# Kernel optimization log

Hardware: AMD Instinct MI355X
Metric: run time of the kernel (lower is better)

Reference implementation:

```python
import jax, jax.numpy as jnp
import numpy as np

NU, NI, D, E_MP, E_UI1, B = 40000, 40000, 128, 640000, 800000, 8192
N = NU + NI

def _segsum(x, ids, n):
    return jax.ops.segment_sum(x, ids, num_segments=n)

def _graph_conv(h, src, dst, n):
    # DGL GraphConv norm='both', weight=None: D_dst^{-1/2} A D_src^{-1/2} h, degrees clamped to >=1
    ones = jnp.ones(src.shape[0], h.dtype)
    outdeg = jnp.maximum(_segsum(ones, src, n), 1.0)
    indeg = jnp.maximum(_segsum(ones, dst, n), 1.0)
    hs = h * jax.lax.rsqrt(outdeg)[:, None]
    agg = _segsum(hs[src], dst, n)  # scatter-add over edges
    return agg * jax.lax.rsqrt(indeg)[:, None]

def _sem_att(z, W1, b1, W2):
    # z: [N, M, D]
    w = jnp.tanh(z @ W1 + b1) @ W2          # [N, M, 1]
    beta = jax.nn.softmax(w.mean(0), axis=0)  # [M, 1]
    return (beta[None] * z).sum(1)            # [N, D]

def _han3(h, mp_edges, W1, b1, W2):
    # 3 applications of the SAME HANLayer (2 metapaths), as in HGCL.forward
    for _ in range(3):
        z = jnp.stack([_graph_conv(h, s, d, h.shape[0]) for (s, d) in mp_edges], axis=1)
        h = _sem_att(z, W1, b1, W2)
    return h

def _ssl(d1, d2, idx):
    e1, e2 = d1[idx], d2[idx]
    n1 = e1 / jnp.maximum(jnp.linalg.norm(e1, axis=1, keepdims=True), 1e-12)
    n2 = e2 / jnp.maximum(jnp.linalg.norm(e2, axis=1, keepdims=True), 1e-12)
    pos = jnp.exp(jnp.sum(n1 * n2, axis=1) / 0.5)
    alls = jnp.sum(jnp.exp(n1 @ n2.T / 0.5), axis=1)
    return -jnp.sum(jnp.log(pos / alls)) / idx.shape[0]

def _layernorm(x, g, b):
    mu = x.mean(-1, keepdims=True)
    var = ((x - mu) ** 2).mean(-1, keepdims=True)
    return (x - mu) * jax.lax.rsqrt(var + 1e-5) * g + b

def setup_inputs():
    key = jax.random.key(0)
    ks = jax.random.split(key, 32)
    f = lambda k, sh, s: jax.random.normal(k, sh, jnp.float32) * s
    ri = lambda k, n, hi: jax.random.randint(k, (n,), 0, hi, dtype=jnp.int32)
    inp = {}
    inp['feat_user'] = f(ks[0], (NU, D), 0.05)
    inp['feat_item'] = f(ks[1], (NI, D), 0.05)
    inp['u_att_W1'] = f(ks[2], (D, 128), 0.05); inp['u_att_b1'] = jnp.zeros((128,), jnp.float32)
    inp['u_att_W2'] = f(ks[3], (128, 1), 0.05)
    inp['i_att_W1'] = f(ks[4], (D, 128), 0.05); inp['i_att_b1'] = jnp.zeros((128,), jnp.float32)
    inp['i_att_W2'] = f(ks[5], (128, 1), 0.05)
    inp['user_W'] = f(ks[6], (D, D), 0.05); inp['user_b'] = jnp.zeros((D,), jnp.float32)
    inp['item_W'] = f(ks[7], (D, D), 0.05); inp['item_b'] = jnp.zeros((D,), jnp.float32)
    inp['ln_g'] = jnp.ones((D,), jnp.float32); inp['ln_b'] = jnp.zeros((D,), jnp.float32)
    # metapath-reachable edge lists (user-user and item-item graphs)
    inp['u_mp0_src'] = ri(ks[8], E_MP, NU); inp['u_mp0_dst'] = ri(ks[9], E_MP, NU)
    inp['u_mp1_src'] = ri(ks[10], E_MP, NU); inp['u_mp1_dst'] = ri(ks[11], E_MP, NU)
    inp['i_mp0_src'] = ri(ks[12], E_MP, NI); inp['i_mp0_dst'] = ri(ks[13], E_MP, NI)
    inp['i_mp1_src'] = ri(ks[14], E_MP, NI); inp['i_mp1_dst'] = ri(ks[15], E_MP, NI)
    # symmetric UI adjacency in COO over N = NU + NI nodes
    ur = ri(ks[16], E_UI1, NU)
    ic = jax.random.randint(ks[17], (E_UI1,), NU, N, dtype=jnp.int32)
    inp['ui_row'] = jnp.concatenate([ur, ic])
    inp['ui_col'] = jnp.concatenate([ic, ur])
    # unique indices (torch.unique in ssl_loss is then a no-op up to ordering)
    inp['user_idx'] = jax.random.permutation(ks[18], NU)[:B]
    inp['item_idx'] = jax.random.permutation(ks[19], NI)[:B]
    inp['neg_item_idx'] = jax.random.permutation(ks[20], NI)[:B]
    return inp

def reference(feat_user, feat_item, u_att_W1, u_att_b1, u_att_W2, i_att_W1, i_att_b1, i_att_W2,
              user_W, user_b, item_W, item_b, ln_g, ln_b,
              u_mp0_src, u_mp0_dst, u_mp1_src, u_mp1_dst,
              i_mp0_src, i_mp0_dst, i_mp1_src, i_mp1_dst,
              ui_row, ui_col, user_idx, item_idx, neg_item_idx):
    h_u = _han3(feat_user, [(u_mp0_src, u_mp0_dst), (u_mp1_src, u_mp1_dst)], u_att_W1, u_att_b1, u_att_W2)
    h_i = _han3(feat_item, [(i_mp0_src, i_mp0_dst), (i_mp1_src, i_mp1_dst)], i_att_W1, i_att_b1, i_att_W2)
    vals = jnp.ones(ui_row.shape[0], jnp.float32)
    deg = _segsum(vals, ui_row, N)
    dinv = jnp.where(deg > 0, jax.lax.rsqrt(jnp.maximum(deg, 1e-30)), 0.0)
    w = dinv[ui_row] * dinv[ui_col]
    x = jnp.concatenate([feat_user, feat_item], axis=0)
    for _ in range(3):
        x = _segsum(w[:, None] * x[ui_col], ui_row, N)
    ui_u, ui_i = x[:NU], x[NU:]
    user_emb = 0.5 * h_u + 0.5 * ui_u
    item_emb = 0.5 * h_i + 0.5 * ui_i
    ssl_loss = 0.4 * _ssl(ui_u, user_emb, user_idx) + 0.4 * _ssl(ui_i, item_emb, item_idx)
    user_emb = _layernorm(jax.nn.relu(user_emb @ user_W + user_b), ln_g, ln_b)
    item_emb = _layernorm(jax.nn.relu(item_emb @ item_W + item_b), ln_g, ln_b)
    return (user_emb[user_idx], item_emb[item_idx], item_emb[neg_item_idx], ssl_loss)
```

## Files before the change

kernel.cpp:

```cpp
#include <hip/hip_runtime.h>
#include <math.h>

typedef unsigned short u16;
typedef unsigned int u32;
typedef unsigned char u8;
typedef __attribute__((ext_vector_type(8))) short bf16x8;
typedef __attribute__((ext_vector_type(4))) float f32x4;

#define CNU 40000
#define CNN 80000
#define CD  128
#define CEMP 640000
#define CEUI 1600000
#define CB  8192

#define BK_CAP 8064
#define P1_CHUNK 4096
#define NB_MP 157

__device__ __forceinline__ float bf2f(u16 b){
  union { u32 u; float f; } v; v.u = ((u32)b) << 16; return v.f;
}
__device__ __forceinline__ u16 f2bf(float f){
  union { float f; u32 u; } v; v.f = f;
  u32 u = v.u + 0x7FFFu + ((v.u >> 16) & 1u);
  return (u16)(u >> 16);
}
__device__ __forceinline__ float lo16f(u32 q){ union { u32 u; float f; } v; v.u = q << 16; return v.f; }
__device__ __forceinline__ float hi16f(u32 q){ union { u32 u; float f; } v; v.u = q & 0xFFFF0000u; return v.f; }

__global__ void k_zero(float* __restrict__ p, long long n){
  long long i = (long long)blockIdx.x*256 + threadIdx.x;
  if (i < n) p[i] = 0.f;
}

__global__ void k_izero(int* __restrict__ p, int n){
  int i = blockIdx.x*256 + threadIdx.x;
  if (i < n) p[i] = 0;
}

__global__ void k_initb(const float* __restrict__ fu, const float* __restrict__ fi,
                        u16* __restrict__ fb,
                        const float* __restrict__ Wu, const float* __restrict__ Wi,
                        u16* __restrict__ Wut, u16* __restrict__ Wit){
  int b = blockIdx.x;
  if (b < 40000){
    int idx = b*256 + threadIdx.x;
    float v = (idx < CNU*CD) ? fu[idx] : fi[idx - CNU*CD];
    fb[idx] = f2bf(v);
  } else {
    int idx = (b - 40000)*256 + threadIdx.x;
    if (idx < 16384){
      int k = idx >> 7, j = idx & 127;
      Wut[j*128 + k] = f2bf(Wu[idx]);
      Wit[j*128 + k] = f2bf(Wi[idx]);
    }
  }
}

__global__ void k_bucket1(const int* __restrict__ src, const int* __restrict__ dst,
                          int* __restrict__ gcur, u32* __restrict__ gpairs,
                          int E, int NB){
  __shared__ int cnt[320];
  __shared__ int sbase[320];
  int t = threadIdx.x;
  for (int i = t; i < NB; i += 256) cnt[i] = 0;
  __syncthreads();
  int base = blockIdx.x * P1_CHUNK;
  int r[16], dv[16], sv[16];
  #pragma unroll
  for (int u = 0; u < 16; ++u){
    int e = base + u*256 + t;
    bool ok = (e < E);
    dv[u] = ok ? dst[e] : -1;
    sv[u] = ok ? src[e] : 0;
    if (ok) r[u] = atomicAdd(&cnt[dv[u] >> 8], 1);
  }
  __syncthreads();
  for (int i = t; i < NB; i += 256){
    int c = cnt[i];
    sbase[i] = c ? atomicAdd(&gcur[i], c) : 0;
  }
  __syncthreads();
  #pragma unroll
  for (int u = 0; u < 16; ++u){
    if (dv[u] >= 0){
      int b = dv[u] >> 8;
      int p = sbase[b] + r[u];
      if (p < BK_CAP)
        gpairs[(long long)b*BK_CAP + p] = (u32)sv[u] | ((u32)(dv[u] & 255) << 18);
    }
  }
}

__global__ void k_bucket1b4(const int* __restrict__ s0, const int* __restrict__ d0,
                            const int* __restrict__ s1, const int* __restrict__ d1,
                            const int* __restrict__ s2, const int* __restrict__ d2,
                            const int* __restrict__ s3, const int* __restrict__ d3,
                            int* __restrict__ gcur, u32* __restrict__ gpairs,
                            int* __restrict__ gcur2, u8* __restrict__ gbytes){
  __shared__ int cnt[320], sbase[320], cnt2[320], sbase2[320];
  int g = blockIdx.y;
  const int* src = (g==0) ? s0 : (g==1) ? s1 : (g==2) ? s2 : s3;
  const int* dst = (g==0) ? d0 : (g==1) ? d1 : (g==2) ? d2 : d3;
  int* gc  = gcur  + g*320;
  int* gc2 = gcur2 + g*320;
  u32* gp  = gpairs + (long long)g*NB_MP*BK_CAP;
  u8*  gb  = gbytes + (long long)g*NB_MP*BK_CAP;
  int t = threadIdx.x;
  for (int i = t; i < NB_MP; i += 256){ cnt[i] = 0; cnt2[i] = 0; }
  __syncthreads();
  int base = blockIdx.x * P1_CHUNK;
  int r[16], r2[16], dv[16], sv[16];
  #pragma unroll
  for (int u = 0; u < 16; ++u){
    int e = base + u*256 + t;
    bool ok = (e < CEMP);
    dv[u] = ok ? dst[e] : -1;
    sv[u] = ok ? src[e] : -1;
    if (ok){
      r[u]  = atomicAdd(&cnt[dv[u] >> 8], 1);
      r2[u] = atomicAdd(&cnt2[sv[u] >> 8], 1);
    }
  }
  __syncthreads();
  for (int i = t; i < NB_MP; i += 256){
    int c  = cnt[i];  sbase[i]  = c  ? atomicAdd(&gc[i],  c)  : 0;
    int c2 = cnt2[i]; sbase2[i] = c2 ? atomicAdd(&gc2[i], c2) : 0;
  }
  __syncthreads();
  #pragma unroll
  for (int u = 0; u < 16; ++u){
    if (dv[u] >= 0){
      int b = dv[u] >> 8;
      int p = sbase[b] + r[u];
      if (p < BK_CAP)
        gp[(long long)b*BK_CAP + p] = (u32)sv[u] | ((u32)(dv[u] & 255) << 18);
      int b2 = sv[u] >> 8;
      int p2 = sbase2[b2] + r2[u];
      if (p2 < BK_CAP)
        gb[(long long)b2*BK_CAP + p2] = (u8)(sv[u] & 255);
    }
  }
}

__global__ void k_scanb(const int* __restrict__ gcur, int* __restrict__ bbase, int NB){
  __shared__ int s[512];
  int g = blockIdx.x;
  const int* gc = gcur + g*320;
  int* bb = bbase + g*320;
  int t = threadIdx.x;
  int v = (t < NB) ? gc[t] : 0;
  s[t] = v;
  __syncthreads();
  for (int off = 1; off < 512; off <<= 1){
    int u = (t >= off) ? s[t-off] : 0;
    __syncthreads();
    s[t] += u;
    __syncthreads();
  }
  if (t < NB) bb[t] = s[t] - v;
}

__global__ void k_odeg4(const u8* __restrict__ gbytes, const int* __restrict__ gcur2,
                        u16* __restrict__ odeg){
  __shared__ int hist[256];
  int g = blockIdx.y;
  int b = blockIdx.x, t = threadIdx.x;
  hist[t] = 0;
  __syncthreads();
  int cnt = gcur2[g*320 + b]; if (cnt > BK_CAP) cnt = BK_CAP;
  const u8* pp = gbytes + (long long)(g*NB_MP + b)*BK_CAP;
  for (int i = t; i < cnt; i += 256) atomicAdd(&hist[pp[i]], 1);
  __syncthreads();
  int dg = (b << 8) + t;
  if (dg < CNU) odeg[g*CNU + dg] = (u16)hist[t];
}

__global__ void k_bucket2(const u32* __restrict__ gpairs, const int* __restrict__ gcur,
                          const int* __restrict__ bbase, int* __restrict__ csr,
                          int* __restrict__ ptr, int n,
                          float* __restrict__ rs_ind, float zval){
  __shared__ int hist[256];
  __shared__ int excl[256];
  __shared__ int lptr[256];
  __shared__ int lsrc[BK_CAP];
  int b = blockIdx.x, t = threadIdx.x;
  int cnt = gcur[b]; if (cnt > BK_CAP) cnt = BK_CAP;
  int base = bbase[b];
  hist[t] = 0;
  __syncthreads();
  const u32* pp = gpairs + (long long)b*BK_CAP;
  for (int i = t; i < cnt; i += 256) atomicAdd(&hist[(pp[i] >> 18) & 255], 1);
  __syncthreads();
  int h = hist[t];
  lptr[t] = h;
  __syncthreads();
  for (int off = 1; off < 256; off <<= 1){
    int u2 = (t >= off) ? lptr[t-off] : 0;
    __syncthreads();
    lptr[t] += u2;
    __syncthreads();
  }
  excl[t] = lptr[t] - h;
  __syncthreads();
  hist[t] = excl[t];
  __syncthreads();
  for (int i = t; i < cnt; i += 256){
    u32 v = pp[i];
    int d = (v >> 18) & 255;
    int p = atomicAdd(&hist[d], 1);
    lsrc[p] = (int)(v & 0x3FFFFu);
  }
  __syncthreads();
  for (int i = t; i < cnt; i += 256) csr[base + i] = lsrc[i];
  int dg = (b << 8) + t;
  if (dg <= n) ptr[dg] = base + excl[t];
  if (dg < n)  rs_ind[dg] = (h > 0) ? rsqrtf((float)h) : zval;
}

__global__ void k_bucket2b4(const u32* __restrict__ gpairs, const int* __restrict__ gcur,
                            const int* __restrict__ bbase, int* __restrict__ csr_base,
                            int* __restrict__ ptr_base, float* __restrict__ rs40k,
                            const u16* __restrict__ odeg){
  __shared__ int hist[256];
  __shared__ int excl[256];
  __shared__ int lptr[256];
  __shared__ int lsrc[BK_CAP];
  int g = blockIdx.y;
  int b = blockIdx.x, t = threadIdx.x;
  int cnt = gcur[g*320 + b]; if (cnt > BK_CAP) cnt = BK_CAP;
  int base = bbase[g*320 + b];
  int* csr = csr_base + (long long)g*CEMP;
  int* ptr = ptr_base + g*(CNU+1);
  float* rs_ind = rs40k + g*80000;
  const u16* od = odeg + g*CNU;
  hist[t] = 0;
  __syncthreads();
  const u32* pp = gpairs + (long long)(g*NB_MP + b)*BK_CAP;
  for (int i = t; i < cnt; i += 256) atomicAdd(&hist[(pp[i] >> 18) & 255], 1);
  __syncthreads();
  int h = hist[t];
  lptr[t] = h;
  __syncthreads();
  for (int off = 1; off < 256; off <<= 1){
    int u2 = (t >= off) ? lptr[t-off] : 0;
    __syncthreads();
    lptr[t] += u2;
    __syncthreads();
  }
  excl[t] = lptr[t] - h;
  __syncthreads();
  hist[t] = excl[t];
  __syncthreads();
  for (int i = t; i < cnt; i += 256){
    u32 v = pp[i];
    int d = (v >> 18) & 255;
    int p = atomicAdd(&hist[d], 1);
    lsrc[p] = (int)(v & 0x3FFFFu);
  }
  __syncthreads();
  for (int i = t; i < cnt; i += 256){
    int s = lsrc[i];
    csr[base + i] = (int)((u32)s | ((u32)od[s] << 16));
  }
  int dg = (b << 8) + t;
  if (dg <= CNU) ptr[dg] = base + excl[t];
  if (dg < CNU)  rs_ind[dg] = (h > 0) ? rsqrtf((float)h) : 1.0f;
}

__global__ void k_gather_mp4(const u16* __restrict__ fb, const u16* __restrict__ hu,
                             const u16* __restrict__ hi, int L,
                             const int* __restrict__ ptr_base, const u32* __restrict__ csr_base,
                             u16* __restrict__ z0base, u16* __restrict__ z2base){
  int row = (blockIdx.x*256 + threadIdx.x) >> 6;
  if (row >= CNU) return;
  int y = blockIdx.y;
  int side = y >> 1;
  const u16* h = (L == 0) ? (fb + (long long)side*CNU*CD) : (side ? hi : hu);
  const int* ptr = ptr_base + y*(CNU+1);
  const u32* csr = csr_base + (long long)y*CEMP;
  u16* z = (y < 2) ? (z0base + (long long)y*CNU*CD) : (z2base + (long long)(y-2)*CNU*CD);
  int lane = threadIdx.x & 63;
  int g = lane >> 4, c = lane & 15;
  int p = ptr[row], pe = ptr[row+1];
  float a0=0,a1=0,a2=0,a3=0,a4=0,a5=0,a6=0,a7=0;
  const u16* hb = h + (long long)c*8;
  int pm = p + ((pe - p) & ~15);
  while (p < pm){
    uint4 q[4]; float w[4];
    #pragma unroll
    for (int u = 0; u < 4; ++u){
      u32 e = csr[p + u*4 + g];
      w[u] = rsqrtf((float)(e >> 16));
      q[u] = *(const uint4*)(hb + (long long)(e & 0xFFFFu)*CD);
    }
    #pragma unroll
    for (int u = 0; u < 4; ++u){
      a0 += lo16f(q[u].x)*w[u]; a1 += hi16f(q[u].x)*w[u];
      a2 += lo16f(q[u].y)*w[u]; a3 += hi16f(q[u].y)*w[u];
      a4 += lo16f(q[u].z)*w[u]; a5 += hi16f(q[u].z)*w[u];
      a6 += lo16f(q[u].w)*w[u]; a7 += hi16f(q[u].w)*w[u];
    }
    p += 16;
  }
  if (p < pe){
    uint4 q[4]; float w[4];
    #pragma unroll
    for (int u = 0; u < 4; ++u){
      int ei = p + u*4 + g;
      bool ok = (ei < pe);
      u32 e = ok ? csr[ei] : 0u;
      w[u] = ok ? rsqrtf((float)(e >> 16)) : 0.f;
      q[u] = *(const uint4*)(hb + (long long)(e & 0xFFFFu)*CD);
    }
    #pragma unroll
    for (int u = 0; u < 4; ++u){
      a0 += lo16f(q[u].x)*w[u]; a1 += hi16f(q[u].x)*w[u];
      a2 += lo16f(q[u].y)*w[u]; a3 += hi16f(q[u].y)*w[u];
      a4 += lo16f(q[u].z)*w[u]; a5 += hi16f(q[u].z)*w[u];
      a6 += lo16f(q[u].w)*w[u]; a7 += hi16f(q[u].w)*w[u];
    }
  }
  #pragma unroll
  for (int m = 16; m <= 32; m <<= 1){
    a0 += __shfl_xor(a0, m); a1 += __shfl_xor(a1, m);
    a2 += __shfl_xor(a2, m); a3 += __shfl_xor(a3, m);
    a4 += __shfl_xor(a4, m); a5 += __shfl_xor(a5, m);
    a6 += __shfl_xor(a6, m); a7 += __shfl_xor(a7, m);
  }
  if (g == 0){
    uint4 o;
    o.x = (u32)f2bf(a0) | ((u32)f2bf(a1) << 16);
    o.y = (u32)f2bf(a2) | ((u32)f2bf(a3) << 16);
    o.z = (u32)f2bf(a4) | ((u32)f2bf(a5) << 16);
    o.w = (u32)f2bf(a6) | ((u32)f2bf(a7) << 16);
    *(uint4*)(z + (long long)row*CD + c*8) = o;
  }
}

__global__ void k_gather_ui(const u16* __restrict__ xin, const int* __restrict__ ptr,
                            const int* __restrict__ csr_src, const float* __restrict__ dinv,
                            u16* __restrict__ xout, int n){
  int row = (blockIdx.x*256 + threadIdx.x) >> 6;
  if (row >= n) return;
  int lane = threadIdx.x & 63;
  int g = lane >> 4, c = lane & 15;
  int p = ptr[row], pe = ptr[row+1];
  float a0=0,a1=0,a2=0,a3=0,a4=0,a5=0,a6=0,a7=0;
  const u16* hb = xin + (long long)c*8;
  int pm = p + ((pe - p) & ~15);
  while (p < pm){
    uint4 q[4]; float w[4];
    #pragma unroll
    for (int u = 0; u < 4; ++u){
      int s = csr_src[p + u*4 + g];
      w[u] = dinv[s];
      q[u] = *(const uint4*)(hb + (long long)s*CD);
    }
    #pragma unroll
    for (int u = 0; u < 4; ++u){
      a0 += lo16f(q[u].x)*w[u]; a1 += hi16f(q[u].x)*w[u];
      a2 += lo16f(q[u].y)*w[u]; a3 += hi16f(q[u].y)*w[u];
      a4 += lo16f(q[u].z)*w[u]; a5 += hi16f(q[u].z)*w[u];
      a6 += lo16f(q[u].w)*w[u]; a7 += hi16f(q[u].w)*w[u];
    }
    p += 16;
  }
  if (p < pe){
    uint4 q[4]; float w[4];
    #pragma unroll
    for (int u = 0; u < 4; ++u){
      int ei = p + u*4 + g;
      bool ok = (ei < pe);
      int s  = ok ? csr_src[ei] : 0;
      w[u]   = ok ? dinv[s] : 0.f;
      q[u]   = *(const uint4*)(hb + (long long)s*CD);
    }
    #pragma unroll
    for (int u = 0; u < 4; ++u){
      a0 += lo16f(q[u].x)*w[u]; a1 += hi16f(q[u].x)*w[u];
      a2 += lo16f(q[u].y)*w[u]; a3 += hi16f(q[u].y)*w[u];
      a4 += lo16f(q[u].z)*w[u]; a5 += hi16f(q[u].z)*w[u];
      a6 += lo16f(q[u].w)*w[u]; a7 += hi16f(q[u].w)*w[u];
    }
  }
  #pragma unroll
  for (int m = 16; m <= 32; m <<= 1){
    a0 += __shfl_xor(a0, m); a1 += __shfl_xor(a1, m);
    a2 += __shfl_xor(a2, m); a3 += __shfl_xor(a3, m);
    a4 += __shfl_xor(a4, m); a5 += __shfl_xor(a5, m);
    a6 += __shfl_xor(a6, m); a7 += __shfl_xor(a7, m);
  }
  if (g == 0){
    float wd = dinv[row];
    uint4 o;
    o.x = (u32)f2bf(a0*wd) | ((u32)f2bf(a1*wd) << 16);
    o.y = (u32)f2bf(a2*wd) | ((u32)f2bf(a3*wd) << 16);
    o.z = (u32)f2bf(a4*wd) | ((u32)f2bf(a5*wd) << 16);
    o.w = (u32)f2bf(a6*wd) | ((u32)f2bf(a7*wd) << 16);
    *(uint4*)(xout + (long long)row*CD + c*8) = o;
  }
}

__global__ void k_att2(const u16* __restrict__ z0, const u16* __restrict__ z1,
                       const u16* __restrict__ z2, const u16* __restrict__ z3,
                       const float* __restrict__ rs40k,
                       const u16* __restrict__ W1Tu, const u16* __restrict__ W1Ti,
                       const float* __restrict__ b1u, const float* __restrict__ b1i,
                       const float* __restrict__ W2u, const float* __restrict__ W2i,
                       float* __restrict__ misc, int L){
  __shared__ float wred[4];
  int side = blockIdx.y;
  const u16* za = side ? z2 : z0;
  const u16* zb = side ? z3 : z1;
  const float* rsi0 = rs40k + side*160000;
  const float* rsi1 = rsi0 + 80000;
  const u16* W1T = side ? W1Ti : W1Tu;
  const float* b1 = side ? b1i : b1u;
  const float* W2 = side ? W2i : W2u;
  float* s_out = misc + side*6 + 2*L;
  int nb = CNU >> 6;
  int blk = blockIdx.x;
  int ch = (blk >= nb) ? 1 : 0;
  int rb = (ch ? (blk - nb) : blk) * 64;
  const u16* z = ch ? zb : za;
  const float* rsi = ch ? rsi1 : rsi0;
  int wv = threadIdx.x >> 6, lane = threadIdx.x & 63;
  int i0 = rb + wv*16;
  int m = lane & 15, kq = lane >> 4;
  bf16x8 a[4];
  #pragma unroll
  for (int t = 0; t < 4; ++t){
    uint4 q = *(const uint4*)(z + (long long)(i0+m)*CD + t*32 + kq*8);
    a[t] = *(bf16x8*)&q;
  }
  float rsv[4];
  #pragma unroll
  for (int ri = 0; ri < 4; ++ri) rsv[ri] = rsi[i0 + kq*4 + ri];
  float psum = 0.f;
  #pragma unroll
  for (int jt = 0; jt < 8; ++jt){
    f32x4 acc = {0.f,0.f,0.f,0.f};
    #pragma unroll
    for (int t = 0; t < 4; ++t){
      uint4 qb = *(const uint4*)(W1T + (jt*16 + m)*CD + t*32 + kq*8);
      bf16x8 b = *(bf16x8*)&qb;
      acc = __builtin_amdgcn_mfma_f32_16x16x32_bf16(a[t], b, acc, 0, 0, 0);
    }
    int j = jt*16 + m;
    float bb = b1[j], w2 = W2[j];
    #pragma unroll
    for (int ri = 0; ri < 4; ++ri){
      float x = acc[ri]*rsv[ri] + bb;
      x = fminf(fmaxf(x, -15.f), 15.f);
      float t2 = __expf(2.f*x);
      psum += ((t2 - 1.f)/(t2 + 1.f))*w2;
    }
  }
  #pragma unroll
  for (int msk = 1; msk <= 32; msk <<= 1) psum += __shfl_xor(psum, msk);
  if (lane == 0) wred[wv] = psum;
  __syncthreads();
  if (threadIdx.x == 0)
    atomicAdd(s_out, wred[0] + wred[1] + wred[2] + wred[3]);
}

__global__ void k_combine2(const u16* __restrict__ z0, const u16* __restrict__ z1,
                           const u16* __restrict__ z2, const u16* __restrict__ z3,
                           const float* __restrict__ rs40k,
                           const float* __restrict__ misc, int L,
                           u16* __restrict__ hu, u16* __restrict__ hi){
  int side = blockIdx.y;
  const u16* za = side ? z2 : z0;
  const u16* zb = side ? z3 : z1;
  const float* rsi0 = rs40k + side*160000;
  const float* rsi1 = rsi0 + 80000;
  const float* s = misc + side*6 + 2*L;
  u16* h = side ? hi : hu;
  int idx = blockIdx.x*256 + threadIdx.x;
  int v = idx >> 7;
  float s0 = s[0]*(1.0f/CNU), s1 = s[1]*(1.0f/CNU);
  float m = fmaxf(s0, s1);
  float e0 = __expf(s0 - m), e1 = __expf(s1 - m);
  float r = 1.0f/(e0 + e1);
  h[idx] = f2bf((e0*r)*bf2f(za[idx])*rsi0[v] + (e1*r)*bf2f(zb[idx])*rsi1[v]);
}

__global__ void k_emb(const u16* __restrict__ x2, u16* __restrict__ h_u,
                      u16* __restrict__ h_i){
  int idx = blockIdx.x*256 + threadIdx.x;
  if (idx >= CNN*CD) return;
  if (idx < CNU*CD) h_u[idx] = f2bf(0.5f*bf2f(h_u[idx]) + 0.5f*bf2f(x2[idx]));
  else { int k = idx - CNU*CD; h_i[k] = f2bf(0.5f*bf2f(h_i[k]) + 0.5f*bf2f(x2[idx])); }
}

__global__ void k_sslnorm2(const u16* __restrict__ x2, const u16* __restrict__ hu,
                           const u16* __restrict__ hi,
                           const int* __restrict__ uidx, const int* __restrict__ iidx,
                           u16* __restrict__ nbase, float* __restrict__ misc){
  __shared__ float wred[4];
  int side = blockIdx.y;
  const int* idx = side ? iidx : uidx;
  const u16* hemb = side ? hi : hu;
  int rowoff = side ? CNU : 0;
  u16* n1b = nbase + (long long)side*2*CB*CD;
  u16* n2b = n1b + (long long)CB*CD;
  float* pos_acc = misc + 12 + 2*side;
  int wv = threadIdx.x >> 6, lane = threadIdx.x & 63;
  int r0 = blockIdx.x*16 + wv*4;
  int g[4]; u32 q1[4], q2[4];
  #pragma unroll
  for (int u = 0; u < 4; ++u){
    g[u] = idx[r0 + u];
    q1[u] = *(const u32*)(x2 + (long long)(g[u] + rowoff)*CD + lane*2);
    q2[u] = *(const u32*)(hemb + (long long)g[u]*CD + lane*2);
  }
  float psum = 0.f;
  #pragma unroll
  for (int u = 0; u < 4; ++u){
    float a0 = lo16f(q1[u]), a1 = hi16f(q1[u]);
    float b0 = lo16f(q2[u]), b1 = hi16f(q2[u]);
    float s1 = a0*a0 + a1*a1, s2 = b0*b0 + b1*b1, s12 = a0*b0 + a1*b1;
    #pragma unroll
    for (int msk = 1; msk <= 32; msk <<= 1){
      s1  += __shfl_xor(s1, msk);
      s2  += __shfl_xor(s2, msk);
      s12 += __shfl_xor(s12, msk);
    }
    float i1 = 1.0f / fmaxf(sqrtf(s1), 1e-12f);
    float i2 = 1.0f / fmaxf(sqrtf(s2), 1e-12f);
    *(u32*)(n1b + (long long)(r0+u)*CD + lane*2) = (u32)f2bf(a0*i1) | ((u32)f2bf(a1*i1) << 16);
    *(u32*)(n2b + (long long)(r0+u)*CD + lane*2) = (u32)f2bf(b0*i2) | ((u32)f2bf(b1*i2) << 16);
    psum += s12*i1*i2*2.0f;
  }
  if (lane == 0) wred[wv] = psum;
  __syncthreads();
  if (threadIdx.x == 0)
    atomicAdd(pos_acc, wred[0] + wred[1] + wred[2] + wred[3]);
}

__global__ void __launch_bounds__(256)
k_alls3(const u16* __restrict__ nbase, float* __restrict__ alls){
  __shared__ uint4 ldsb[2][256];
  int side = blockIdx.z;
  const u16* n1b = nbase + (long long)side*2*CB*CD;
  const u16* n2b = n1b + (long long)CB*CD;
  float* al = alls + side*CB;
  int wv = threadIdx.x >> 6, lane = threadIdx.x & 63;
  int m = lane & 15, kq = lane >> 4;
  int i0 = (blockIdx.x*8 + wv*2)*16;
  bf16x8 a[2][4];
  #pragma unroll
  for (int c = 0; c < 2; ++c){
    #pragma unroll
    for (int t = 0; t < 4; ++t){
      uint4 q = *(const uint4*)(n1b + (long long)(i0 + c*16 + m)*CD + t*32 + kq*8);
      a[c][t] = *(bf16x8*)&q;
    }
  }
  float es0[4] = {0.f,0.f,0.f,0.f};
  float es1[4] = {0.f,0.f,0.f,0.f};
  int j0 = blockIdx.y*512;
  int sr = threadIdx.x >> 4, sc = threadIdx.x & 15;
  const u16* sp = n2b + (long long)(j0 + sr)*CD + sc*8;
  int se = sr*16 + (sc ^ (sr & 7));
  uint4 v = *(const uint4*)sp;
  for (int jt = 0; jt < 32; ++jt){
    ldsb[jt & 1][se] = v;
    if (jt < 31) v = *(const uint4*)(sp + (long long)(jt+1)*16*CD);
    __syncthreads();
    f32x4 ac0 = {0.f,0.f,0.f,0.f}, ac1 = {0.f,0.f,0.f,0.f};
    #pragma unroll
    for (int t = 0; t < 4; ++t){
      int cc = 4*t + kq;
      uint4 bq = ldsb[jt & 1][m*16 + (cc ^ (m & 7))];
      bf16x8 b = *(bf16x8*)&bq;
      ac0 = __builtin_amdgcn_mfma_f32_16x16x32_bf16(a[0][t], b, ac0, 0, 0, 0);
      ac1 = __builtin_amdgcn_mfma_f32_16x16x32_bf16(a[1][t], b, ac1, 0, 0, 0);
    }
    #pragma unroll
    for (int ri = 0; ri < 4; ++ri){
      es0[ri] += __expf(ac0[ri]*2.f);
      es1[ri] += __expf(ac1[ri]*2.f);
    }
  }
  #pragma unroll
  for (int ri = 0; ri < 4; ++ri){
    float v0 = es0[ri], v1 = es1[ri];
    #pragma unroll
    for (int msk = 1; msk <= 8; msk <<= 1){
      v0 += __shfl_xor(v0, msk);
      v1 += __shfl_xor(v1, msk);
    }
    if (m == 0){
      atomicAdd(&al[i0 + kq*4 + ri], v0);
      atomicAdd(&al[i0 + 16 + kq*4 + ri], v1);
    }
  }
}

__global__ void k_logsum(const float* __restrict__ alls, float* __restrict__ misc){
  int i = blockIdx.x*256 + threadIdx.x;
  float v = logf(alls[i]);
  for (int off = 32; off > 0; off >>= 1) v += __shfl_down(v, off);
  if ((threadIdx.x & 63) == 0) atomicAdd(&misc[(i < CB) ? 13 : 15], v);
}

__global__ void k_final3(const u16* __restrict__ hu, const u16* __restrict__ hi,
                         const int* __restrict__ uidx, const int* __restrict__ iidx,
                         const int* __restrict__ nidx,
                         const float* __restrict__ uW, const float* __restrict__ ub,
                         const float* __restrict__ iW, const float* __restrict__ ib,
                         const float* __restrict__ lg, const float* __restrict__ lb,
                         float* __restrict__ outp){
  __shared__ float A[8][128];
  __shared__ float red[8][4];
  int y = blockIdx.y;
  const u16* emb = (y == 0) ? hu : hi;
  const int* idx = (y == 0) ? uidx : ((y == 1) ? iidx : nidx);
  const float* W = (y == 0) ? uW : iW;
  const float* bias = (y == 0) ? ub : ib;
  float* outb = outp + (long long)y*CB*CD;
  int j = threadIdx.x;
  int r0 = blockIdx.x*8;
  for (int r = 0; r < 8; ++r){
    int g = idx[r0 + r];
    A[r][j] = bf2f(emb[(long long)g*CD + j]);
  }
  __syncthreads();
  float acc[8];
  #pragma unroll
  for (int r = 0; r < 8; ++r) acc[r] = 0.f;
  for (int k = 0; k < 128; k += 4){
    float w0 = W[(k+0)*128 + j];
    float w1 = W[(k+1)*128 + j];
    float w2 = W[(k+2)*128 + j];
    float w3 = W[(k+3)*128 + j];
    #pragma unroll
    for (int r = 0; r < 8; ++r){
      float4 a = *(const float4*)&A[r][k];
      acc[r] += a.x*w0 + a.y*w1 + a.z*w2 + a.w*w3;
    }
  }
  float bb = bias[j];
  #pragma unroll
  for (int r = 0; r < 8; ++r){
    float v = acc[r] + bb;
    acc[r] = (v < 0.f) ? 0.f : v;
  }
  int wid = j >> 6, lane = j & 63;
  #pragma unroll
  for (int r = 0; r < 8; ++r){
    float s = acc[r], q = acc[r]*acc[r];
    for (int off = 32; off > 0; off >>= 1){
      s += __shfl_down(s, off); q += __shfl_down(q, off);
    }
    if (lane == 0){ red[r][wid*2] = s; red[r][wid*2+1] = q; }
  }
  __syncthreads();
  float gg = lg[j], be = lb[j];
  #pragma unroll
  for (int r = 0; r < 8; ++r){
    float mu = (red[r][0] + red[r][2]) * (1.0f/128.0f);
    float ms = (red[r][1] + red[r][3]) * (1.0f/128.0f);
    float var = ms - mu*mu;
    float yv = (acc[r] - mu) * rsqrtf(var + 1e-5f) * gg + be;
    outb[(long long)(r0 + r)*CD + j] = yv;
  }
}

__global__ void k_loss(const float* __restrict__ misc, float* __restrict__ o){
  float lu = (misc[13] - misc[12]) * (1.0f/CB);
  float li = (misc[15] - misc[14]) * (1.0f/CB);
  o[0] = 0.4f*(lu + li);
}

extern "C" void kernel_launch(void* const* d_in, const int* in_sizes, int n_in,
                              void* d_out, int out_size, void* d_ws, size_t ws_size,
                              hipStream_t stream){
  (void)in_sizes; (void)n_in; (void)out_size; (void)ws_size;
  const float* feat_user = (const float*)d_in[0];
  const float* feat_item = (const float*)d_in[1];
  const float* u_W1 = (const float*)d_in[2];
  const float* u_b1 = (const float*)d_in[3];
  const float* u_W2 = (const float*)d_in[4];
  const float* i_W1 = (const float*)d_in[5];
  const float* i_b1 = (const float*)d_in[6];
  const float* i_W2 = (const float*)d_in[7];
  const float* user_W = (const float*)d_in[8];
  const float* user_b = (const float*)d_in[9];
  const float* item_W = (const float*)d_in[10];
  const float* item_b = (const float*)d_in[11];
  const float* ln_g = (const float*)d_in[12];
  const float* ln_b = (const float*)d_in[13];
  const int* ump0s = (const int*)d_in[14]; const int* ump0d = (const int*)d_in[15];
  const int* ump1s = (const int*)d_in[16]; const int* ump1d = (const int*)d_in[17];
  const int* imp0s = (const int*)d_in[18]; const int* imp0d = (const int*)d_in[19];
  const int* imp1s = (const int*)d_in[20]; const int* imp1d = (const int*)d_in[21];
  const int* ui_row = (const int*)d_in[22]; const int* ui_col = (const int*)d_in[23];
  const int* user_idx = (const int*)d_in[24]; const int* item_idx = (const int*)d_in[25];
  const int* neg_idx = (const int*)d_in[26];

  u16* W  = (u16*)d_ws;
  u16* fb = W;
  u16* hu = W + 10240000LL;
  u16* hi = W + 15360000LL;
  u16* xb = W + 20480000LL;
  u16* x2 = W + 30720000LL;
  u16* z0 = W + 40960000LL;
  u16* z1 = W + 46080000LL;
  float* F   = (float*)(W + 51200000LL);
  float* rs  = F;
  float* dinv= F + 320000;
  float* alls= F + 400000;
  float* misc= F + 416384;
  int* I     = (int*)(F + 416448);
  int* mp_p  = I;
  int* gcur  = I + 160004;
  int* bbase = I + 161284;
  int* gcur2 = I + 162564;
  int* mp_c  = I + 163844;
  u16* w1tu  = (u16*)(I + 2723844);
  u16* w1ti  = w1tu + 16384;
  int* ui_ptr    = (int*)hu;
  int* ui_csr    = ui_ptr + 160001;
  u32* gpairsU   = (u32*)z0;
  u32* gpairs4   = (u32*)z0;
  u8*  gbytes4   = (u8*)xb;
  u16* odeg4     = xb + 2540000LL;
  u16* z2 = xb;
  u16* z3 = xb + 5120000LL;
  u16* nbase = xb;
  float* out = (float*)d_out;

  k_zero<<<(16448 + 255)/256, 256, 0, stream>>>(alls, 16448);
  k_initb<<<40064, 256, 0, stream>>>(feat_user, feat_item, fb, u_W1, i_W1, w1tu, w1ti);

  k_izero<<<15, 256, 0, stream>>>(gcur, 3840);
  k_bucket1<<<(CEUI + P1_CHUNK - 1)/P1_CHUNK, 256, 0, stream>>>(ui_col, ui_row, gcur, gpairsU, CEUI, 313);
  k_scanb<<<1, 512, 0, stream>>>(gcur, bbase, 313);
  k_bucket2<<<313, 256, 0, stream>>>(gpairsU, gcur, bbase, ui_csr, ui_ptr, CNN, dinv, 0.0f);

  k_gather_ui<<<20000, 256, 0, stream>>>(fb, ui_ptr, ui_csr, dinv, x2, CNN);
  k_gather_ui<<<20000, 256, 0, stream>>>(x2, ui_ptr, ui_csr, dinv, xb, CNN);
  k_gather_ui<<<20000, 256, 0, stream>>>(xb, ui_ptr, ui_csr, dinv, x2, CNN);

  k_izero<<<15, 256, 0, stream>>>(gcur, 3840);
  k_bucket1b4<<<dim3((CEMP + P1_CHUNK - 1)/P1_CHUNK, 4), 256, 0, stream>>>(
      ump0s, ump0d, ump1s, ump1d, imp0s, imp0d, imp1s, imp1d,
      gcur, gpairs4, gcur2, gbytes4);
  k_scanb<<<4, 512, 0, stream>>>(gcur, bbase, NB_MP);
  k_odeg4<<<dim3(NB_MP, 4), 256, 0, stream>>>(gbytes4, gcur2, odeg4);
  k_bucket2b4<<<dim3(NB_MP, 4), 256, 0, stream>>>(gpairs4, gcur, bbase, mp_c, mp_p, rs + 40000, odeg4);

  for (int L = 0; L < 3; ++L){
    k_gather_mp4<<<dim3(10000, 4), 256, 0, stream>>>(fb, hu, hi, L, mp_p, (const u32*)mp_c, z0, z2);
    k_att2<<<dim3(1250, 2), 256, 0, stream>>>(z0, z1, z2, z3, rs + 40000,
                                              w1tu, w1ti, u_b1, i_b1, u_W2, i_W2, misc, L);
    k_combine2<<<dim3(20000, 2), 256, 0, stream>>>(z0, z1, z2, z3, rs + 40000, misc, L, hu, hi);
  }

  k_emb<<<40000, 256, 0, stream>>>(x2, hu, hi);

  k_sslnorm2<<<dim3(CB/16, 2), 256, 0, stream>>>(x2, hu, hi, user_idx, item_idx, nbase, misc);
  k_alls3<<<dim3(64, 16, 2), 256, 0, stream>>>(nbase, alls);
  k_logsum<<<64, 256, 0, stream>>>(alls, misc);

  k_final3<<<dim3(1024, 3), 128, 0, stream>>>(hu, hi, user_idx, item_idx, neg_idx,
                                              user_W, user_b, item_W, item_b,
                                              ln_g, ln_b, out);
  k_loss<<<1, 1, 0, stream>>>(misc, out + 3LL*CB*CD);
}
```

Before: 1.035 ms.

## Stage attention weights in LDS with multi-tile reuse; vectorize elementwise kernels

The attention-score kernel now loads the transposed W1 into swizzled shared memory once per block. Each wave processes four 16-row tiles, so every B fragment feeds four MFMAs. This replaces the repeated global loads of W1 per 16 rows, at the cost of more registers and fewer, larger blocks. The bf16 init, combine and embedding-average kernels are also rewritten to handle 8 elements per thread with 128-bit loads and stores, which cuts the thread count and instruction overhead of these memory-bound passes.

```diff
diff --git a/kernel.cpp b/kernel.cpp
--- a/kernel.cpp
+++ b/kernel.cpp
@@ -28,6 +28,9 @@
 }
 __device__ __forceinline__ float lo16f(u32 q){ union { u32 u; float f; } v; v.u = q << 16; return v.f; }
 __device__ __forceinline__ float hi16f(u32 q){ union { u32 u; float f; } v; v.u = q & 0xFFFF0000u; return v.f; }
+__device__ __forceinline__ u32 pack2(float a, float b){
+  return (u32)f2bf(a) | ((u32)f2bf(b) << 16);
+}
 
 __global__ void k_zero(float* __restrict__ p, long long n){
   long long i = (long long)blockIdx.x*256 + threadIdx.x;
@@ -44,12 +47,19 @@
                         const float* __restrict__ Wu, const float* __restrict__ Wi,
                         u16* __restrict__ Wut, u16* __restrict__ Wit){
   int b = blockIdx.x;
-  if (b < 40000){
-    int idx = b*256 + threadIdx.x;
-    float v = (idx < CNU*CD) ? fu[idx] : fi[idx - CNU*CD];
-    fb[idx] = f2bf(v);
+  if (b < 5000){
+    long long off = ((long long)b*256 + threadIdx.x)*8;
+    const float* src = (off < (long long)CNU*CD) ? (fu + off) : (fi + (off - (long long)CNU*CD));
+    float4 f0 = *(const float4*)src;
+    float4 f1 = *(const float4*)(src + 4);
+    uint4 o;
+    o.x = pack2(f0.x, f0.y);
+    o.y = pack2(f0.z, f0.w);
+    o.z = pack2(f1.x, f1.y);
+    o.w = pack2(f1.z, f1.w);
+    *(uint4*)(fb + off) = o;
   } else {
-    int idx = (b - 40000)*256 + threadIdx.x;
+    int idx = (b - 5000)*256 + threadIdx.x;
     if (idx < 16384){
       int k = idx >> 7, j = idx & 127;
       Wut[j*128 + k] = f2bf(Wu[idx]);
@@ -331,10 +341,10 @@
   }
   if (g == 0){
     uint4 o;
-    o.x = (u32)f2bf(a0) | ((u32)f2bf(a1) << 16);
-    o.y = (u32)f2bf(a2) | ((u32)f2bf(a3) << 16);
-    o.z = (u32)f2bf(a4) | ((u32)f2bf(a5) << 16);
-    o.w = (u32)f2bf(a6) | ((u32)f2bf(a7) << 16);
+    o.x = pack2(a0, a1);
+    o.y = pack2(a2, a3);
+    o.z = pack2(a4, a5);
+    o.w = pack2(a6, a7);
     *(uint4*)(z + (long long)row*CD + c*8) = o;
   }
 }
@@ -395,82 +405,96 @@
   if (g == 0){
     float wd = dinv[row];
     uint4 o;
-    o.x = (u32)f2bf(a0*wd) | ((u32)f2bf(a1*wd) << 16);
-    o.y = (u32)f2bf(a2*wd) | ((u32)f2bf(a3*wd) << 16);
-    o.z = (u32)f2bf(a4*wd) | ((u32)f2bf(a5*wd) << 16);
-    o.w = (u32)f2bf(a6*wd) | ((u32)f2bf(a7*wd) << 16);
+    o.x = pack2(a0*wd, a1*wd);
+    o.y = pack2(a2*wd, a3*wd);
+    o.z = pack2(a4*wd, a5*wd);
+    o.w = pack2(a6*wd, a7*wd);
     *(uint4*)(xout + (long long)row*CD + c*8) = o;
   }
 }
 
-__global__ void k_att2(const u16* __restrict__ z0, const u16* __restrict__ z1,
-                       const u16* __restrict__ z2, const u16* __restrict__ z3,
-                       const float* __restrict__ rs40k,
-                       const u16* __restrict__ W1Tu, const u16* __restrict__ W1Ti,
-                       const float* __restrict__ b1u, const float* __restrict__ b1i,
-                       const float* __restrict__ W2u, const float* __restrict__ W2i,
-                       float* __restrict__ misc, int L){
+__global__ void __launch_bounds__(256)
+k_att3(const u16* __restrict__ z0, const u16* __restrict__ z1,
+       const u16* __restrict__ z2, const u16* __restrict__ z3,
+       const float* __restrict__ rs40k,
+       const u16* __restrict__ W1Tu, const u16* __restrict__ W1Ti,
+       const float* __restrict__ b1u, const float* __restrict__ b1i,
+       const float* __restrict__ W2u, const float* __restrict__ W2i,
+       float* __restrict__ misc, int L){
+  __shared__ uint4 ldsW[2048];
   __shared__ float wred[4];
-  int side = blockIdx.y;
-  const u16* za = side ? z2 : z0;
-  const u16* zb = side ? z3 : z1;
-  const float* rsi0 = rs40k + side*160000;
-  const float* rsi1 = rsi0 + 80000;
+  int side = blockIdx.z, ch = blockIdx.y;
+  const u16* z = side ? (ch ? z3 : z2) : (ch ? z1 : z0);
+  const float* rsi = rs40k + side*160000 + ch*80000;
   const u16* W1T = side ? W1Ti : W1Tu;
   const float* b1 = side ? b1i : b1u;
   const float* W2 = side ? W2i : W2u;
-  float* s_out = misc + side*6 + 2*L;
-  int nb = CNU >> 6;
-  int blk = blockIdx.x;
-  int ch = (blk >= nb) ? 1 : 0;
-  int rb = (ch ? (blk - nb) : blk) * 64;
-  const u16* z = ch ? zb : za;
-  const float* rsi = ch ? rsi1 : rsi0;
-  int wv = threadIdx.x >> 6, lane = threadIdx.x & 63;
-  int i0 = rb + wv*16;
+  float* s_out = misc + side*6 + 2*L + ch;
+  int t = threadIdx.x;
+  for (int i = t; i < 2048; i += 256){
+    int row = i >> 4, c = i & 15;
+    ldsW[(row << 4) | (c ^ (row & 7))] = *(const uint4*)(W1T + row*CD + c*8);
+  }
+  __syncthreads();
+  int wv = t >> 6, lane = t & 63;
   int m = lane & 15, kq = lane >> 4;
-  bf16x8 a[4];
-  #pragma unroll
-  for (int t = 0; t < 4; ++t){
-    uint4 q = *(const uint4*)(z + (long long)(i0+m)*CD + t*32 + kq*8);
-    a[t] = *(bf16x8*)&q;
-  }
-  float rsv[4];
-  #pragma unroll
-  for (int ri = 0; ri < 4; ++ri) rsv[ri] = rsi[i0 + kq*4 + ri];
+  int base = blockIdx.x*256 + wv*64;
   float psum = 0.f;
-  #pragma unroll
-  for (int jt = 0; jt < 8; ++jt){
-    f32x4 acc = {0.f,0.f,0.f,0.f};
-    #pragma unroll
-    for (int t = 0; t < 4; ++t){
-      uint4 qb = *(const uint4*)(W1T + (jt*16 + m)*CD + t*32 + kq*8);
-      bf16x8 b = *(bf16x8*)&qb;
-      acc = __builtin_amdgcn_mfma_f32_16x16x32_bf16(a[t], b, acc, 0, 0, 0);
-    }
-    int j = jt*16 + m;
-    float bb = b1[j], w2 = W2[j];
-    #pragma unroll
-    for (int ri = 0; ri < 4; ++ri){
-      float x = acc[ri]*rsv[ri] + bb;
-      x = fminf(fmaxf(x, -15.f), 15.f);
-      float t2 = __expf(2.f*x);
-      psum += ((t2 - 1.f)/(t2 + 1.f))*w2;
-    }
-  }
-  #pragma unroll
-  for (int msk = 1; msk <= 32; msk <<= 1) psum += __shfl_xor(psum, msk);
+  if (base < CNU){
+    bf16x8 a[4][4];
+    float rsv[4][4];
+    #pragma unroll
+    for (int c = 0; c < 4; ++c){
+      int row = base + c*16;
+      #pragma unroll
+      for (int tt = 0; tt < 4; ++tt){
+        uint4 q = *(const uint4*)(z + (long long)(row + m)*CD + tt*32 + kq*8);
+        a[c][tt] = *(bf16x8*)&q;
+      }
+      #pragma unroll
+      for (int ri = 0; ri < 4; ++ri) rsv[c][ri] = rsi[row + kq*4 + ri];
+    }
+    #pragma unroll
+    for (int jt = 0; jt < 8; ++jt){
+      f32x4 acc[4];
+      #pragma unroll
+      for (int c = 0; c < 4; ++c) acc[c] = (f32x4){0.f,0.f,0.f,0.f};
+      #pragma unroll
+      for (int tt = 0; tt < 4; ++tt){
+        int row = jt*16 + m;
+        uint4 bq = ldsW[(row << 4) | ((tt*4 + kq) ^ (row & 7))];
+        bf16x8 b = *(bf16x8*)&bq;
+        #pragma unroll
+        for (int c = 0; c < 4; ++c)
+          acc[c] = __builtin_amdgcn_mfma_f32_16x16x32_bf16(a[c][tt], b, acc[c], 0, 0, 0);
+      }
+      int j = jt*16 + m;
+      float bb = b1[j], w2 = W2[j];
+      #pragma unroll
+      for (int c = 0; c < 4; ++c){
+        #pragma unroll
+        for (int ri = 0; ri < 4; ++ri){
+          float x = acc[c][ri]*rsv[c][ri] + bb;
+          x = fminf(fmaxf(x, -15.f), 15.f);
+          float t2 = __expf(2.f*x);
+          psum += ((t2 - 1.f)/(t2 + 1.f))*w2;
+        }
+      }
+    }
+    #pragma unroll
+    for (int msk = 1; msk <= 32; msk <<= 1) psum += __shfl_xor(psum, msk);
+  }
   if (lane == 0) wred[wv] = psum;
   __syncthreads();
-  if (threadIdx.x == 0)
+  if (t == 0)
     atomicAdd(s_out, wred[0] + wred[1] + wred[2] + wred[3]);
 }
 
-__global__ void k_combine2(const u16* __restrict__ z0, const u16* __restrict__ z1,
-                           const u16* __restrict__ z2, const u16* __restrict__ z3,
-                           const float* __restrict__ rs40k,
-                           const float* __restrict__ misc, int L,
-                           u16* __restrict__ hu, u16* __restrict__ hi){
+__global__ void k_combine2v(const u16* __restrict__ z0, const u16* __restrict__ z1,
+                            const u16* __restrict__ z2, const u16* __restrict__ z3,
+                            const float* __restrict__ rs40k,
+                            const float* __restrict__ misc, int L,
+                            u16* __restrict__ hu, u16* __restrict__ hi){
   int side = blockIdx.y;
   const u16* za = side ? z2 : z0;
   const u16* zb = side ? z3 : z1;
@@ -478,21 +502,37 @@
   const float* rsi1 = rsi0 + 80000;
   const float* s = misc + side*6 + 2*L;
   u16* h = side ? hi : hu;
-  int idx = blockIdx.x*256 + threadIdx.x;
-  int v = idx >> 7;
+  long long off = ((long long)blockIdx.x*256 + threadIdx.x)*8;
+  int v = (int)(off >> 7);
   float s0 = s[0]*(1.0f/CNU), s1 = s[1]*(1.0f/CNU);
   float m = fmaxf(s0, s1);
   float e0 = __expf(s0 - m), e1 = __expf(s1 - m);
   float r = 1.0f/(e0 + e1);
-  h[idx] = f2bf((e0*r)*bf2f(za[idx])*rsi0[v] + (e1*r)*bf2f(zb[idx])*rsi1[v]);
-}
-
-__global__ void k_emb(const u16* __restrict__ x2, u16* __restrict__ h_u,
-                      u16* __restrict__ h_i){
-  int idx = blockIdx.x*256 + threadIdx.x;
-  if (idx >= CNN*CD) return;
-  if (idx < CNU*CD) h_u[idx] = f2bf(0.5f*bf2f(h_u[idx]) + 0.5f*bf2f(x2[idx]));
-  else { int k = idx - CNU*CD; h_i[k] = f2bf(0.5f*bf2f(h_i[k]) + 0.5f*bf2f(x2[idx])); }
+  float wa = (e0*r)*rsi0[v], wb = (e1*r)*rsi1[v];
+  uint4 qa = *(const uint4*)(za + off);
+  uint4 qb = *(const uint4*)(zb + off);
+  uint4 o;
+  o.x = pack2(lo16f(qa.x)*wa + lo16f(qb.x)*wb, hi16f(qa.x)*wa + hi16f(qb.x)*wb);
+  o.y = pack2(lo16f(qa.y)*wa + lo16f(qb.y)*wb, hi16f(qa.y)*wa + hi16f(qb.y)*wb);
+  o.z = pack2(lo16f(qa.z)*wa + lo16f(qb.z)*wb, hi16f(qa.z)*wa + hi16f(qb.z)*wb);
+  o.w = pack2(lo16f(qa.w)*wa + lo16f(qb.w)*wb, hi16f(qa.w)*wa + hi16f(qb.w)*wb);
+  *(uint4*)(h + off) = o;
+}
+
+__global__ void k_embv(const u16* __restrict__ x2, u16* __restrict__ h_u,
+                       u16* __restrict__ h_i){
+  long long off = ((long long)blockIdx.x*256 + threadIdx.x)*8;
+  u16* h; long long ho;
+  if (off < (long long)CNU*CD){ h = h_u; ho = off; }
+  else { h = h_i; ho = off - (long long)CNU*CD; }
+  uint4 qx = *(const uint4*)(x2 + off);
+  uint4 qh = *(const uint4*)(h + ho);
+  uint4 o;
+  o.x = pack2(0.5f*bf2f((u16)(qh.x & 0xFFFF)) + 0.5f*lo16f(qx.x), 0.5f*hi16f(qh.x) + 0.5f*hi16f(qx.x));
+  o.y = pack2(0.5f*lo16f(qh.y) + 0.5f*lo16f(qx.y), 0.5f*hi16f(qh.y) + 0.5f*hi16f(qx.y));
+  o.z = pack2(0.5f*lo16f(qh.z) + 0.5f*lo16f(qx.z), 0.5f*hi16f(qh.z) + 0.5f*hi16f(qx.z));
+  o.w = pack2(0.5f*lo16f(qh.w) + 0.5f*lo16f(qx.w), 0.5f*hi16f(qh.w) + 0.5f*hi16f(qx.w));
+  *(uint4*)(h + ho) = o;
 }
 
 __global__ void k_sslnorm2(const u16* __restrict__ x2, const u16* __restrict__ hu,
@@ -530,8 +570,8 @@
     }
     float i1 = 1.0f / fmaxf(sqrtf(s1), 1e-12f);
     float i2 = 1.0f / fmaxf(sqrtf(s2), 1e-12f);
-    *(u32*)(n1b + (long long)(r0+u)*CD + lane*2) = (u32)f2bf(a0*i1) | ((u32)f2bf(a1*i1) << 16);
-    *(u32*)(n2b + (long long)(r0+u)*CD + lane*2) = (u32)f2bf(b0*i2) | ((u32)f2bf(b1*i2) << 16);
+    *(u32*)(n1b + (long long)(r0+u)*CD + lane*2) = pack2(a0*i1, a1*i1);
+    *(u32*)(n2b + (long long)(r0+u)*CD + lane*2) = pack2(b0*i2, b1*i2);
     psum += s12*i1*i2*2.0f;
   }
   if (lane == 0) wred[wv] = psum;
@@ -735,7 +775,7 @@
   float* out = (float*)d_out;
 
   k_zero<<<(16448 + 255)/256, 256, 0, stream>>>(alls, 16448);
-  k_initb<<<40064, 256, 0, stream>>>(feat_user, feat_item, fb, u_W1, i_W1, w1tu, w1ti);
+  k_initb<<<5064, 256, 0, stream>>>(feat_user, feat_item, fb, u_W1, i_W1, w1tu, w1ti);
 
   k_izero<<<15, 256, 0, stream>>>(gcur, 3840);
   k_bucket1<<<(CEUI + P1_CHUNK - 1)/P1_CHUNK, 256, 0, stream>>>(ui_col, ui_row, gcur, gpairsU, CEUI, 313);
@@ -756,12 +796,12 @@
 
   for (int L = 0; L < 3; ++L){
     k_gather_mp4<<<dim3(10000, 4), 256, 0, stream>>>(fb, hu, hi, L, mp_p, (const u32*)mp_c, z0, z2);
-    k_att2<<<dim3(1250, 2), 256, 0, stream>>>(z0, z1, z2, z3, rs + 40000,
-                                              w1tu, w1ti, u_b1, i_b1, u_W2, i_W2, misc, L);
-    k_combine2<<<dim3(20000, 2), 256, 0, stream>>>(z0, z1, z2, z3, rs + 40000, misc, L, hu, hi);
-  }
-
-  k_emb<<<40000, 256, 0, stream>>>(x2, hu, hi);
+    k_att3<<<dim3(157, 2, 2), 256, 0, stream>>>(z0, z1, z2, z3, rs + 40000,
+                                                w1tu, w1ti, u_b1, i_b1, u_W2, i_W2, misc, L);
+    k_combine2v<<<dim3(2500, 2), 256, 0, stream>>>(z0, z1, z2, z3, rs + 40000, misc, L, hu, hi);
+  }
+
+  k_embv<<<5000, 256, 0, stream>>>(x2, hu, hi);
 
   k_sslnorm2<<<dim3(CB/16, 2), 256, 0, stream>>>(x2, hu, hi, user_idx, item_idx, nbase, misc);
   k_alls3<<<dim3(64, 16, 2), 256, 0, stream>>>(nbase, alls);
```

New measurement: 864.8 us. -16.5%, faster.
